# Optimization experiments

Hardware: AMD Instinct MI355X
Metric: run time of the kernel (lower is better)

The kernel has to match this reference:

```python
import jax, jax.numpy as jnp
import numpy as np

N_SRC = 50000
N_DST = 50000
E = 800000
D = 128
OUT = 128


def setup_inputs() -> dict:
    key = jax.random.key(0)
    k1, k2, k3, k4, k5, k6 = jax.random.split(key, 6)
    lim = 1.0 / np.sqrt(D)
    return {
        "x_src": jax.random.normal(k1, (N_SRC, D), dtype=jnp.float32),
        "x_dst": jax.random.normal(k2, (N_DST, D), dtype=jnp.float32),
        "edge_src": jax.random.randint(k3, (E,), 0, N_SRC, dtype=jnp.int64),
        "edge_dst": jax.random.randint(k4, (E,), 0, N_DST, dtype=jnp.int64),
        "num_dst": N_DST,
        # learned params (torch nn.Linear: y = x @ W.T + b), stored here as [in, out]
        "W_neigh": jax.random.uniform(k5, (D, OUT), jnp.float32, -lim, lim),
        "b_neigh": jnp.zeros((OUT,), jnp.float32),
        "W_self": jax.random.uniform(k6, (D, OUT), jnp.float32, -lim, lim),
        "b_self": jnp.zeros((OUT,), jnp.float32),
    }


def reference(x_src, x_dst, edge_src, edge_dst, num_dst, W_neigh, b_neigh, W_self, b_self):
    # gather source features per edge: [E, D]
    neigh_feats = x_src[edge_src]
    # scatter-mean onto destination nodes
    summed = jax.ops.segment_sum(neigh_feats, edge_dst, num_segments=num_dst)  # [num_dst, D]
    count = jax.ops.segment_sum(jnp.ones((edge_dst.shape[0], 1), x_src.dtype), edge_dst,
                                num_segments=num_dst)
    agg = summed / jnp.clip(count, 1.0)
    # dual linear + add
    return agg @ W_neigh + b_neigh + x_dst @ W_self + b_self
```

## Files before the change

### kernel.cpp

```cpp
#include <hip/hip_runtime.h>

#define D 128
#define TM 64
#define CBITS 7
#define CSIZE 128
#define MAXNB 512
#define CAPB 2560

typedef __attribute__((ext_vector_type(8))) short bf16x8;
typedef __attribute__((ext_vector_type(4))) float f32x4;


__device__ __forceinline__ unsigned short f32_to_bf16(float x) {
    unsigned u = __float_as_uint(x);
    u += 0x7FFFu + ((u >> 16) & 1u);
    return (unsigned short)(u >> 16);
}
__device__ __forceinline__ float bf16_to_f32(unsigned short h) {
    return __uint_as_float(((unsigned)h) << 16);
}

__global__ __launch_bounds__(256) void prep_kernel(
    const float* __restrict__ Wn, const float* __restrict__ Ws,
    unsigned short* __restrict__ Wtn, unsigned short* __restrict__ Wts,
    int* __restrict__ gcursor, int NB) {
    const int stride = gridDim.x * 256;
    for (int i = blockIdx.x * 256 + threadIdx.x; i < D * D; i += stride) {
        int n = i >> 7, k = i & (D - 1);
        Wtn[i] = f32_to_bf16(Wn[k * D + n]);
        Wts[i] = f32_to_bf16(Ws[k * D + n]);
    }
    for (int i = blockIdx.x * 256 + threadIdx.x; i < NB; i += stride)
        gcursor[i] = 0;
}

__global__ __launch_bounds__(256) void fused_part_gemm_kernel(
    const int* __restrict__ edge_src, const int* __restrict__ edge_dst,
    int* __restrict__ gcursor, int* __restrict__ packed, int E, int NB,
    const float* __restrict__ x_src, const float* __restrict__ x_dst,
    const unsigned short* __restrict__ Wtn, const unsigned short* __restrict__ Wts,
    const float* __restrict__ bn, const float* __restrict__ bs,
    unsigned short* __restrict__ y16, float* __restrict__ out,
    int M_SRC, int N, int nblk, int blkA) {
    __shared__ __align__(16) char smem[TM * 136 * 2 + D * 136 * 2];
    const int t = threadIdx.x;

    if ((int)blockIdx.x < nblk) {
        int* lh    = (int*)smem;
        int* lbase = lh + MAXNB;
        for (int i = t; i < NB; i += 256) lh[i] = 0;
        __syncthreads();
        const int base = blockIdx.x * 2048;
        int es[8], ed[8];
        #pragma unroll
        for (int i = 0; i < 8; ++i) {
            int idx = base + t + i * 256;
            if (idx < E) { es[i] = edge_src[idx]; ed[i] = edge_dst[idx]; }
            else ed[i] = -1;
        }
        #pragma unroll
        for (int i = 0; i < 8; ++i)
            if (ed[i] >= 0) atomicAdd(&lh[ed[i] >> CBITS], 1);
        __syncthreads();
        for (int i = t; i < NB; i += 256) {
            int v = lh[i];
            lbase[i] = v ? atomicAdd(&gcursor[i], v) : 0;
        }
        __syncthreads();
        for (int i = t; i < NB; i += 256) lh[i] = 0;
        __syncthreads();
        #pragma unroll
        for (int i = 0; i < 8; ++i) {
            if (ed[i] >= 0) {
                int bk = ed[i] >> CBITS;
                int pos = lbase[bk] + atomicAdd(&lh[bk], 1);
                if (pos < CAPB)
                    packed[(size_t)bk * CAPB + pos] =
                        (es[i] << CBITS) | (ed[i] & (CSIZE - 1));
            }
        }
        return;
    }

    typedef unsigned short ushort136[136];
    ushort136* LA = (ushort136*)smem;
    ushort136* LW = (ushort136*)(smem + TM * 136 * 2);

    const int  gb   = (int)blockIdx.x - nblk;
    const bool isA  = gb < blkA;
    const int  row0 = (isA ? gb : gb - blkA) * TM;
    const int  M    = isA ? M_SRC : N;
    const float* Ap = isA ? x_src : x_dst;
    const unsigned short* Wp = isA ? Wtn : Wts;

    {
        const float4* Av = (const float4*)Ap;
        #pragma unroll
        for (int i = 0; i < 8; ++i) {
            int vi = t + i * 256;
            int r = vi >> 5, c4 = vi & 31;
            int sr = min(row0 + r, M - 1);
            float4 v = Av[(size_t)sr * 32 + c4];
            ushort4 p;
            p.x = f32_to_bf16(v.x); p.y = f32_to_bf16(v.y);
            p.z = f32_to_bf16(v.z); p.w = f32_to_bf16(v.w);
            *(ushort4*)&LA[r][c4 * 4] = p;
        }
        const int4* Wv = (const int4*)Wp;
        #pragma unroll
        for (int i = 0; i < 8; ++i) {
            int vi = t + i * 256;
            int r = vi >> 4, c8 = vi & 15;
            *(int4*)&LW[r][c8 * 8] = Wv[vi];
        }
    }
    __syncthreads();

    const int lane = t & 63;
    const int wv   = t >> 6;
    const int m0   = wv * 16;
    const int lr   = lane & 15;
    const int g    = lane >> 4;

    f32x4 acc[8];
    #pragma unroll
    for (int n = 0; n < 8; ++n) acc[n] = (f32x4){0.f, 0.f, 0.f, 0.f};

    #pragma unroll
    for (int kt = 0; kt < 4; ++kt) {
        bf16x8 a = *(const bf16x8*)&LA[m0 + lr][kt * 32 + g * 8];
        #pragma unroll
        for (int n = 0; n < 8; ++n) {
            bf16x8 b = *(const bf16x8*)&LW[n * 16 + lr][kt * 32 + g * 8];
            acc[n] = __builtin_amdgcn_mfma_f32_16x16x32_bf16(a, b, acc[n], 0, 0, 0);
        }
    }

    if (isA) {
        #pragma unroll
        for (int n = 0; n < 8; ++n) {
            #pragma unroll
            for (int r = 0; r < 4; ++r) {
                int row = row0 + m0 + g * 4 + r;
                if (row < M) y16[(size_t)row * D + n * 16 + lr] = f32_to_bf16(acc[n][r]);
            }
        }
    } else {
        #pragma unroll
        for (int n = 0; n < 8; ++n) {
            int col = n * 16 + lr;
            float bias = bn[col] + bs[col];
            #pragma unroll
            for (int r = 0; r < 4; ++r) {
                int row = row0 + m0 + g * 4 + r;
                if (row < M) out[(size_t)row * D + col] = acc[n][r] + bias;
            }
        }
    }
}

__global__ __launch_bounds__(256) void fine_kernel(
    const int* __restrict__ packed, const int* __restrict__ gcursor,
    int* __restrict__ off_beg, int* __restrict__ off_end,
    int* __restrict__ eidx, int N) {
    __shared__ int dcount[CSIZE];
    __shared__ int dbase[CSIZE];
    __shared__ int sbuf[CSIZE];
    const int b  = blockIdx.x;
    const int d0 = b << CBITS;
    const int beg = b * CAPB;
    const int cnt = min(gcursor[b], CAPB);
    const int t = threadIdx.x;
    if (t < CSIZE) dcount[t] = 0;
    __syncthreads();
    for (int i = t; i < cnt; i += 256)
        atomicAdd(&dcount[packed[beg + i] & (CSIZE - 1)], 1);
    __syncthreads();
    if (t < CSIZE) sbuf[t] = dcount[t];
    __syncthreads();
    for (int ofs = 1; ofs < CSIZE; ofs <<= 1) {
        int u = (t < CSIZE && t >= ofs) ? sbuf[t - ofs] : 0;
        __syncthreads();
        if (t < CSIZE) sbuf[t] += u;
        __syncthreads();
    }
    if (t < CSIZE) {
        int excl = sbuf[t] - dcount[t];
        dbase[t] = excl;
        int d = d0 + t;
        if (d < N) {
            off_beg[d] = beg + excl;
            off_end[d] = beg + excl + dcount[t];
        }
    }
    __syncthreads();
    if (t < CSIZE) dcount[t] = dbase[t];
    __syncthreads();
    for (int i = t; i < cnt; i += 256) {
        int p = packed[beg + i];
        int pos = beg + atomicAdd(&dcount[p & (CSIZE - 1)], 1);
        eidx[pos] = p >> CBITS;
    }
}

__global__ void gather_out_kernel(const unsigned short* __restrict__ y16,
                                  const int* __restrict__ off_beg,
                                  const int* __restrict__ off_end,
                                  const int* __restrict__ eidx,
                                  float* __restrict__ out, int N) {
    const int wave = (int)(((long long)blockIdx.x * blockDim.x + threadIdx.x) >> 6);
    const int lane = threadIdx.x & 63;
    if (wave >= N) return;
    const int h = lane >> 4;
    const int c = lane & 15;
    const int beg = off_beg[wave];
    const int end = off_end[wave];

    float acc[8];
    #pragma unroll
    for (int j = 0; j < 8; ++j) acc[j] = 0.f;

    for (int i = beg + h; i < end; i += 4) {
        int s = eidx[i];
        const int4 v = *reinterpret_cast<const int4*>(y16 + (size_t)s * D + c * 8);
        const unsigned short* hs = (const unsigned short*)&v;
        #pragma unroll
        for (int j = 0; j < 8; ++j) acc[j] += bf16_to_f32(hs[j]);
    }

    #pragma unroll
    for (int j = 0; j < 8; ++j) {
        acc[j] += __shfl_down(acc[j], 32);
        acc[j] += __shfl_down(acc[j], 16);
    }

    if (h == 0) {
        const float inv = 1.0f / fmaxf((float)(end - beg), 1.0f);
        float4* o = reinterpret_cast<float4*>(out + (size_t)wave * D) + c * 2;
        float4 c0 = o[0], c1 = o[1];
        c0.x = fmaf(acc[0], inv, c0.x);
        c0.y = fmaf(acc[1], inv, c0.y);
        c0.z = fmaf(acc[2], inv, c0.z);
        c0.w = fmaf(acc[3], inv, c0.w);
        c1.x = fmaf(acc[4], inv, c1.x);
        c1.y = fmaf(acc[5], inv, c1.y);
        c1.z = fmaf(acc[6], inv, c1.z);
        c1.w = fmaf(acc[7], inv, c1.w);
        o[0] = c0;
        o[1] = c1;
    }
}

extern "C" void kernel_launch(void* const* d_in, const int* in_sizes, int n_in,
                              void* d_out, int out_size, void* d_ws, size_t ws_size,
                              hipStream_t stream) {
    const float* x_src    = (const float*)d_in[0];
    const float* x_dst    = (const float*)d_in[1];
    const int*   edge_src = (const int*)d_in[2];
    const int*   edge_dst = (const int*)d_in[3];
    const float* Wn = (const float*)d_in[5];
    const float* bn = (const float*)d_in[6];
    const float* Ws = (const float*)d_in[7];
    const float* bs = (const float*)d_in[8];

    const int E     = in_sizes[2];
    const int N     = in_sizes[1] / D;
    const int M_SRC = in_sizes[0] / D;

    const int NB   = (N + CSIZE - 1) >> CBITS;
    const int nblk = (E + 2047) / 2048;

    unsigned short* y16 = (unsigned short*)d_ws;
    unsigned short* Wtn = y16 + (size_t)M_SRC * D;
    unsigned short* Wts = Wtn + D * D;
    int* packed  = (int*)(Wts + D * D);
    int* eidx    = packed + (size_t)NB * CAPB;
    int* off_beg = eidx + (size_t)NB * CAPB;
    int* off_end = off_beg + N;
    int* gcursor = off_end + N;

    const int T = 256;
    prep_kernel<<<32, T, 0, stream>>>(Wn, Ws, Wtn, Wts, gcursor, NB);

    const int blkA = (M_SRC + TM - 1) / TM;
    const int blkB = (N + TM - 1) / TM;
    fused_part_gemm_kernel<<<nblk + blkA + blkB, T, 0, stream>>>(
        edge_src, edge_dst, gcursor, packed, E, NB,
        x_src, x_dst, Wtn, Wts, bn, bs, y16, (float*)d_out,
        M_SRC, N, nblk, blkA);

    fine_kernel<<<NB, T, 0, stream>>>(packed, gcursor, off_beg, off_end, eidx, N);

    gather_out_kernel<<<(N + 3) / 4, T, 0, stream>>>(
        y16, off_beg, off_end, eidx, (float*)d_out, N);
}
```

Before: 86.75 us.

## Interleave partition blocks among GEMM blocks and use 2x4 wave MFMA tiling

Partition (bucketing) blocks are now spread evenly through the grid at a fixed stride rather than all launched first, so atomic-heavy partition work and the compute-heavy GEMM tiles run side by side on the CUs. The GEMM per-wave tiling changes from 16 rows by 128 columns to 32 rows by 64 columns, which cuts B-fragment LDS reads per MFMA by reusing two A fragments against four B fragments. The block-id to role mapping becomes more complex and relies on the stride arithmetic being correct.

```diff
diff --git a/kernel.cpp b/kernel.cpp
--- a/kernel.cpp
+++ b/kernel.cpp
@@ -41,21 +41,25 @@
     const unsigned short* __restrict__ Wtn, const unsigned short* __restrict__ Wts,
     const float* __restrict__ bn, const float* __restrict__ bs,
     unsigned short* __restrict__ y16, float* __restrict__ out,
-    int M_SRC, int N, int nblk, int blkA) {
+    int M_SRC, int N, int nblk, int blkA, int pstride) {
     __shared__ __align__(16) char smem[TM * 136 * 2 + D * 136 * 2];
     const int t = threadIdx.x;
-
-    if ((int)blockIdx.x < nblk) {
+    const int idx = (int)blockIdx.x;
+
+    const bool isPart = (idx % pstride == 0) && (idx / pstride < nblk);
+
+    if (isPart) {
+        const int pid = idx / pstride;
         int* lh    = (int*)smem;
         int* lbase = lh + MAXNB;
         for (int i = t; i < NB; i += 256) lh[i] = 0;
         __syncthreads();
-        const int base = blockIdx.x * 2048;
+        const int base = pid * 2048;
         int es[8], ed[8];
         #pragma unroll
         for (int i = 0; i < 8; ++i) {
-            int idx = base + t + i * 256;
-            if (idx < E) { es[i] = edge_src[idx]; ed[i] = edge_dst[idx]; }
+            int e = base + t + i * 256;
+            if (e < E) { es[i] = edge_src[e]; ed[i] = edge_dst[e]; }
             else ed[i] = -1;
         }
         #pragma unroll
@@ -86,7 +90,8 @@
     ushort136* LA = (ushort136*)smem;
     ushort136* LW = (ushort136*)(smem + TM * 136 * 2);
 
-    const int  gb   = (int)blockIdx.x - nblk;
+    const int npb  = min((idx + pstride - 1) / pstride, nblk);
+    const int gb   = idx - npb;
     const bool isA  = gb < blkA;
     const int  row0 = (isA ? gb : gb - blkA) * TM;
     const int  M    = isA ? M_SRC : N;
@@ -118,42 +123,62 @@
 
     const int lane = t & 63;
     const int wv   = t >> 6;
-    const int m0   = wv * 16;
+    const int wr   = wv & 1;
+    const int wc   = wv >> 1;
     const int lr   = lane & 15;
     const int g    = lane >> 4;
 
-    f32x4 acc[8];
+    f32x4 acc[2][4];
     #pragma unroll
-    for (int n = 0; n < 8; ++n) acc[n] = (f32x4){0.f, 0.f, 0.f, 0.f};
+    for (int i = 0; i < 2; ++i)
+        #pragma unroll
+        for (int j = 0; j < 4; ++j) acc[i][j] = (f32x4){0.f, 0.f, 0.f, 0.f};
 
     #pragma unroll
     for (int kt = 0; kt < 4; ++kt) {
-        bf16x8 a = *(const bf16x8*)&LA[m0 + lr][kt * 32 + g * 8];
-        #pragma unroll
-        for (int n = 0; n < 8; ++n) {
-            bf16x8 b = *(const bf16x8*)&LW[n * 16 + lr][kt * 32 + g * 8];
-            acc[n] = __builtin_amdgcn_mfma_f32_16x16x32_bf16(a, b, acc[n], 0, 0, 0);
-        }
+        bf16x8 b0 = *(const bf16x8*)&LW[wc * 64 + 0 * 16 + lr][kt * 32 + g * 8];
+        bf16x8 b1 = *(const bf16x8*)&LW[wc * 64 + 1 * 16 + lr][kt * 32 + g * 8];
+        bf16x8 b2 = *(const bf16x8*)&LW[wc * 64 + 2 * 16 + lr][kt * 32 + g * 8];
+        bf16x8 b3 = *(const bf16x8*)&LW[wc * 64 + 3 * 16 + lr][kt * 32 + g * 8];
+        bf16x8 a0 = *(const bf16x8*)&LA[wr * 32 + lr][kt * 32 + g * 8];
+        bf16x8 a1 = *(const bf16x8*)&LA[wr * 32 + 16 + lr][kt * 32 + g * 8];
+        acc[0][0] = __builtin_amdgcn_mfma_f32_16x16x32_bf16(a0, b0, acc[0][0], 0, 0, 0);
+        acc[0][1] = __builtin_amdgcn_mfma_f32_16x16x32_bf16(a0, b1, acc[0][1], 0, 0, 0);
+        acc[0][2] = __builtin_amdgcn_mfma_f32_16x16x32_bf16(a0, b2, acc[0][2], 0, 0, 0);
+        acc[0][3] = __builtin_amdgcn_mfma_f32_16x16x32_bf16(a0, b3, acc[0][3], 0, 0, 0);
+        acc[1][0] = __builtin_amdgcn_mfma_f32_16x16x32_bf16(a1, b0, acc[1][0], 0, 0, 0);
+        acc[1][1] = __builtin_amdgcn_mfma_f32_16x16x32_bf16(a1, b1, acc[1][1], 0, 0, 0);
+        acc[1][2] = __builtin_amdgcn_mfma_f32_16x16x32_bf16(a1, b2, acc[1][2], 0, 0, 0);
+        acc[1][3] = __builtin_amdgcn_mfma_f32_16x16x32_bf16(a1, b3, acc[1][3], 0, 0, 0);
     }
 
     if (isA) {
         #pragma unroll
-        for (int n = 0; n < 8; ++n) {
+        for (int i = 0; i < 2; ++i) {
             #pragma unroll
-            for (int r = 0; r < 4; ++r) {
-                int row = row0 + m0 + g * 4 + r;
-                if (row < M) y16[(size_t)row * D + n * 16 + lr] = f32_to_bf16(acc[n][r]);
+            for (int j = 0; j < 4; ++j) {
+                int col = wc * 64 + j * 16 + lr;
+                #pragma unroll
+                for (int r = 0; r < 4; ++r) {
+                    int row = row0 + wr * 32 + i * 16 + g * 4 + r;
+                    if (row < M)
+                        y16[(size_t)row * D + col] = f32_to_bf16(acc[i][j][r]);
+                }
             }
         }
     } else {
         #pragma unroll
-        for (int n = 0; n < 8; ++n) {
-            int col = n * 16 + lr;
-            float bias = bn[col] + bs[col];
+        for (int i = 0; i < 2; ++i) {
             #pragma unroll
-            for (int r = 0; r < 4; ++r) {
-                int row = row0 + m0 + g * 4 + r;
-                if (row < M) out[(size_t)row * D + col] = acc[n][r] + bias;
+            for (int j = 0; j < 4; ++j) {
+                int col = wc * 64 + j * 16 + lr;
+                float bias = bn[col] + bs[col];
+                #pragma unroll
+                for (int r = 0; r < 4; ++r) {
+                    int row = row0 + wr * 32 + i * 16 + g * 4 + r;
+                    if (row < M)
+                        out[(size_t)row * D + col] = acc[i][j][r] + bias;
+                }
             }
         }
     }
@@ -284,10 +309,12 @@
 
     const int blkA = (M_SRC + TM - 1) / TM;
     const int blkB = (N + TM - 1) / TM;
-    fused_part_gemm_kernel<<<nblk + blkA + blkB, T, 0, stream>>>(
+    const int total = nblk + blkA + blkB;
+    const int pstride = total / nblk > 1 ? total / nblk : 1;
+    fused_part_gemm_kernel<<<total, T, 0, stream>>>(
         edge_src, edge_dst, gcursor, packed, E, NB,
         x_src, x_dst, Wtn, Wts, bn, bs, y16, (float*)d_out,
-        M_SRC, N, nblk, blkA);
+        M_SRC, N, nblk, blkA, pstride);
 
     fine_kernel<<<NB, T, 0, stream>>>(packed, gcursor, off_beg, off_end, eidx, N);
 
```

Result: faster. 77.79 us (-10.3%).
